# Kernel tuning notes

Hardware: AMD Instinct MI355X
Metric: run time of the kernel (lower is better)

Reference implementation:

```python
import jax, jax.numpy as jnp
import numpy as np

B, KPLUS1, D = 64, 513, 1024

def setup_inputs() -> dict:
    key = jax.random.key(0)
    k1, k2, k3 = jax.random.split(key, 3)
    x = jax.random.normal(k1, (B, KPLUS1, D), dtype=jnp.float32)
    # glorot-style scaled init for faithfulness in magnitude
    dense_weights = jax.random.normal(k2, (2 * D, D), dtype=jnp.float32) * (1.0 / np.sqrt(2 * D))
    dot_bias = jax.random.normal(k3, (D, 1), dtype=jnp.float32) * (1.0 / np.sqrt(D))
    return {"x": x, "dense_weights": dense_weights, "dot_bias": dot_bias}

def reference(x, dense_weights, dot_bias):
    # x: [B, K+1, D]; x[:,0] = sentence encoding u, x[:,1:] = knowledge z_t
    u = x[:, 0, :]            # [B, D]
    z = x[:, 1:, :]           # [B, K, D]
    d = z.shape[-1]
    # concat(z_t, u) @ W1 == z @ W1[:D] + u @ W1[D:], broadcast over K
    # (mathematically identical to the tile+concat+matmul in the original)
    w_z = dense_weights[:d, :]   # [D, D]
    w_u = dense_weights[d:, :]   # [D, D]
    m = jnp.tanh(jnp.einsum('bkd,de->bke', z, w_z)
                 + jnp.einsum('bd,de->be', u, w_u)[:, None, :])  # [B, K, D]
    q = jnp.einsum('bke,e->bk', m, dot_bias[:, 0])               # [B, K]
    return jax.nn.softmax(q, axis=-1)                            # [B, K]
```

## Files before the change

### kernel.cpp

```cpp
#include <hip/hip_runtime.h>
#include <hip/hip_bf16.h>


typedef __attribute__((ext_vector_type(8))) short short8;
typedef __attribute__((ext_vector_type(8))) _Float16 half8;
typedef __attribute__((ext_vector_type(4))) float f32x4;
typedef unsigned short ushort_t;

typedef const __attribute__((address_space(1))) void gvoid_t;
typedef __attribute__((address_space(3))) void lvoid_t;

__device__ __forceinline__ ushort_t f2bf(float f) {
    unsigned u = __float_as_uint(f);
    unsigned r = u + 0x7FFFu + ((u >> 16) & 1u);
    return (ushort_t)(r >> 16);
}
__device__ __forceinline__ float bf2f(ushort_t h) {
    return __uint_as_float(((unsigned)h) << 16);
}
__device__ __forceinline__ float tanh_fast(float x) {
    float e = __expf(2.f * x);
    return 1.f - 2.f / (e + 1.f);
}

__global__ __launch_bounds__(256) void k_prep_z16(const float* __restrict__ x,
                                                  _Float16* __restrict__ z_h) {
    const int idx8 = blockIdx.x * 256 + threadIdx.x;
    const int m = idx8 >> 7;
    const int c = (idx8 & 127) * 8;
    const int b = m >> 9, k = m & 511;
    const float* src = x + ((size_t)(b * 513 + 1 + k) << 10) + c;
    const float4 v0 = *(const float4*)src;
    const float4 v1 = *(const float4*)(src + 4);
    float vv[8] = {v0.x, v0.y, v0.z, v0.w, v1.x, v1.y, v1.z, v1.w};
    half8 hv;
#pragma unroll
    for (int i = 0; i < 8; ++i) hv[i] = (_Float16)vv[i];
    *(half8*)(z_h + (size_t)m * 1024 + c) = hv;
}

__global__ void k_prep_w16(const float* __restrict__ w,
                           _Float16* __restrict__ wzt) {
    __shared__ _Float16 th[64][66];
    const int k0 = blockIdx.x * 64;
    const int n0 = blockIdx.y * 64;
    const int t = threadIdx.x;
    const int lr = t >> 6;
    const int lc = t & 63;
#pragma unroll
    for (int r = 0; r < 16; ++r) {
        int kk = r * 4 + lr;
        th[kk][lc] = (_Float16)w[(size_t)(k0 + kk) * 1024 + n0 + lc];
    }
    __syncthreads();
#pragma unroll
    for (int r = 0; r < 16; ++r) {
        int nn = r * 4 + lr;
        wzt[(size_t)(n0 + nn) * 1024 + k0 + lc] = th[lc][nn];
    }
}

__global__ void k_hu(const float* __restrict__ x,
                     const float* __restrict__ w,
                     float* __restrict__ hu) {
    __shared__ float us[1024];
    const int b = blockIdx.y;
    const int e = blockIdx.x * 256 + threadIdx.x;
    for (int i = threadIdx.x; i < 1024; i += 256)
        us[i] = x[(size_t)b * 513 * 1024 + i];
    __syncthreads();
    const float* wu = w + (size_t)1024 * 1024;
    float acc = 0.f;
#pragma unroll 8
    for (int d = 0; d < 1024; ++d)
        acc = fmaf(us[d], wu[(size_t)d * 1024 + e], acc);
    hu[b * 1024 + e] = acc;
}

__global__ __launch_bounds__(512, 2) void k_gemm9(
        const _Float16* __restrict__ z_h,
        const _Float16* __restrict__ wzt,
        const float* __restrict__ hu,
        const float* __restrict__ bias,
        float* __restrict__ qp) {
    __shared__ __align__(16) _Float16 As[256 * 64];
    __shared__ __align__(16) _Float16 Bs[256 * 64];
    __shared__ float qred[2][4][128];

    const int t = threadIdx.x;
    const int mtile = blockIdx.x;
    const int ntile = blockIdx.y;
    const int wid = t >> 6;
    const int l = t & 63;
    const int wm = wid >> 2;
    const int wn = wid & 3;
    const int lr = l & 15;
    const int g = l >> 4;

    const int rl = l >> 3;
    const int chunk = (l & 7) ^ rl;
    const int w4 = wid & 3;
    const _Float16* gsrc;
    _Float16* ldsT;
    if (wid < 4) {
        gsrc = z_h + (size_t)(mtile * 256 + w4 * 64 + rl) * 1024 + chunk * 8;
        ldsT = As + w4 * 4096;
    } else {
        gsrc = wzt + (size_t)(ntile * 256 + w4 * 64 + rl) * 1024 + chunk * 8;
        ldsT = Bs + w4 * 4096;
    }

    f32x4 acc[8][4] = {};

    for (int k0 = 0; k0 < 1024; k0 += 64) {
#pragma unroll
        for (int j = 0; j < 8; ++j) {
            __builtin_amdgcn_global_load_lds(
                (gvoid_t*)(gsrc + k0 + j * 8192),
                (lvoid_t*)((char*)ldsT + j * 1024 + l * 16),
                16, 0, 0);
        }
        __syncthreads();

#pragma unroll
        for (int ks = 0; ks < 2; ++ks) {
            half8 afr[8], bfr[4];
            const int so = ((ks * 4 + g) ^ (lr & 7)) * 16;
#pragma unroll
            for (int ni = 0; ni < 4; ++ni)
                bfr[ni] = *(const half8*)((const char*)Bs + (wn * 64 + ni * 16 + lr) * 128 + so);
#pragma unroll
            for (int mi = 0; mi < 8; ++mi)
                afr[mi] = *(const half8*)((const char*)As + (wm * 128 + mi * 16 + lr) * 128 + so);
#pragma unroll
            for (int mi = 0; mi < 8; ++mi)
#pragma unroll
                for (int ni = 0; ni < 4; ++ni)
                    acc[mi][ni] = __builtin_amdgcn_mfma_f32_16x16x32_f16(
                        afr[mi], bfr[ni], acc[mi][ni], 0, 0, 0);
        }
        __syncthreads();
    }

    const int bb = mtile >> 1;
    float hu4[4], bias4[4];
#pragma unroll
    for (int ni = 0; ni < 4; ++ni) {
        int e = ntile * 256 + wn * 64 + ni * 16 + lr;
        hu4[ni] = hu[bb * 1024 + e];
        bias4[ni] = bias[e];
    }
#pragma unroll
    for (int mi = 0; mi < 8; ++mi) {
#pragma unroll
        for (int j = 0; j < 4; ++j) {
            float v = 0.f;
#pragma unroll
            for (int ni = 0; ni < 4; ++ni)
                v += tanh_fast(acc[mi][ni][j] + hu4[ni]) * bias4[ni];
            v += __shfl_xor(v, 1);
            v += __shfl_xor(v, 2);
            v += __shfl_xor(v, 4);
            v += __shfl_xor(v, 8);
            if (lr == 0)
                qred[wm][wn][mi * 16 + g * 4 + j] = v;
        }
    }
    __syncthreads();
    if (t < 256) {
        const int wmr = t >> 7;
        const int rr = t & 127;
        float q = qred[wmr][0][rr] + qred[wmr][1][rr]
                + qred[wmr][2][rr] + qred[wmr][3][rr];
        qp[(size_t)ntile * 32768 + mtile * 256 + t] = q;
    }
}

__global__ void k_prep_w(const float* __restrict__ w,
                         ushort_t* __restrict__ wzt_hi,
                         ushort_t* __restrict__ wzt_lo) {
    __shared__ ushort_t th[64][66];
    __shared__ ushort_t tl[64][66];
    const int k0 = blockIdx.x * 64;
    const int n0 = blockIdx.y * 64;
    const int t = threadIdx.x;
    const int lr = t >> 6;
    const int lc = t & 63;
#pragma unroll
    for (int r = 0; r < 16; ++r) {
        int kk = r * 4 + lr;
        float f = w[(size_t)(k0 + kk) * 1024 + n0 + lc];
        ushort_t hi = f2bf(f);
        ushort_t lo = f2bf(f - bf2f(hi));
        th[kk][lc] = hi;
        tl[kk][lc] = lo;
    }
    __syncthreads();
#pragma unroll
    for (int r = 0; r < 16; ++r) {
        int nn = r * 4 + lr;
        wzt_hi[(size_t)(n0 + nn) * 1024 + k0 + lc] = th[lc][nn];
        wzt_lo[(size_t)(n0 + nn) * 1024 + k0 + lc] = tl[lc][nn];
    }
}

__global__ __launch_bounds__(256) void k_gemm(
        const float* __restrict__ x,
        const ushort_t* __restrict__ wzt_hi,
        const ushort_t* __restrict__ wzt_lo,
        const float* __restrict__ hu,
        const float* __restrict__ bias,
        float* __restrict__ qp) {
    __shared__ ushort_t As_hi[128][40];
    __shared__ ushort_t As_lo[128][40];
    __shared__ ushort_t Bs_hi[128][40];
    __shared__ ushort_t Bs_lo[128][40];
    __shared__ float qred[2][2][64];

    const int t = threadIdx.x;
    const int mtile = blockIdx.x;
    const int ntile = blockIdx.y;
    const int wid = t >> 6;
    const int l = t & 63;
    const int wm = wid >> 1;
    const int wn = wid & 1;

    f32x4 acc[4][4] = {};

    const int arow = t >> 3;
    const int acol = (t & 7) * 4;
    size_t abase[4];
#pragma unroll
    for (int it = 0; it < 4; ++it) {
        int m = mtile * 128 + arow + it * 32;
        int bb = m >> 9;
        int kk = m & 511;
        abase[it] = ((size_t)(bb * 513 + 1 + kk)) * 1024 + acol;
    }
    const int brow = t >> 2;
    const int bcol = (t & 3) * 8;
    const size_t bbase = (size_t)(ntile * 128 + brow) * 1024 + bcol;

    for (int k0 = 0; k0 < 1024; k0 += 32) {
#pragma unroll
        for (int it = 0; it < 4; ++it) {
            const float4 v = *(const float4*)(x + abase[it] + k0);
            ushort4 hv, lv;
            hv.x = f2bf(v.x); lv.x = f2bf(v.x - bf2f(hv.x));
            hv.y = f2bf(v.y); lv.y = f2bf(v.y - bf2f(hv.y));
            hv.z = f2bf(v.z); lv.z = f2bf(v.z - bf2f(hv.z));
            hv.w = f2bf(v.w); lv.w = f2bf(v.w - bf2f(hv.w));
            const int row = arow + it * 32;
            *(ushort4*)&As_hi[row][acol] = hv;
            *(ushort4*)&As_lo[row][acol] = lv;
        }
#pragma unroll
        for (int it = 0; it < 2; ++it) {
            const int row = brow + it * 64;
            const uint4 vh = *(const uint4*)(wzt_hi + bbase + (size_t)it * 64 * 1024 + k0);
            const uint4 vl = *(const uint4*)(wzt_lo + bbase + (size_t)it * 64 * 1024 + k0);
            *(uint4*)&Bs_hi[row][bcol] = vh;
            *(uint4*)&Bs_lo[row][bcol] = vl;
        }
        __syncthreads();

        const int lr = l & 15;
        const int lk = (l >> 4) * 8;
        short8 ah[4], al[4], bh[4], bl[4];
#pragma unroll
        for (int i = 0; i < 4; ++i) {
            ah[i] = *(const short8*)&As_hi[wm * 64 + i * 16 + lr][lk];
            al[i] = *(const short8*)&As_lo[wm * 64 + i * 16 + lr][lk];
            bh[i] = *(const short8*)&Bs_hi[wn * 64 + i * 16 + lr][lk];
            bl[i] = *(const short8*)&Bs_lo[wn * 64 + i * 16 + lr][lk];
        }
#pragma unroll
        for (int mi = 0; mi < 4; ++mi)
#pragma unroll
            for (int ni = 0; ni < 4; ++ni) {
                acc[mi][ni] = __builtin_amdgcn_mfma_f32_16x16x32_bf16(ah[mi], bh[ni], acc[mi][ni], 0, 0, 0);
                acc[mi][ni] = __builtin_amdgcn_mfma_f32_16x16x32_bf16(ah[mi], bl[ni], acc[mi][ni], 0, 0, 0);
                acc[mi][ni] = __builtin_amdgcn_mfma_f32_16x16x32_bf16(al[mi], bh[ni], acc[mi][ni], 0, 0, 0);
            }
        __syncthreads();
    }

    const int lr = l & 15;
    const int lg = l >> 4;
    const int bbatch = mtile >> 2;
    float hu4[4], bias4[4];
#pragma unroll
    for (int ni = 0; ni < 4; ++ni) {
        int e = ntile * 128 + wn * 64 + ni * 16 + lr;
        hu4[ni] = hu[bbatch * 1024 + e];
        bias4[ni] = bias[e];
    }
#pragma unroll
    for (int mi = 0; mi < 4; ++mi) {
#pragma unroll
        for (int j = 0; j < 4; ++j) {
            float v = 0.f;
#pragma unroll
            for (int ni = 0; ni < 4; ++ni)
                v += tanhf(acc[mi][ni][j] + hu4[ni]) * bias4[ni];
            v += __shfl_xor(v, 1);
            v += __shfl_xor(v, 2);
            v += __shfl_xor(v, 4);
            v += __shfl_xor(v, 8);
            if (lr == 0)
                qred[wm][wn][mi * 16 + lg * 4 + j] = v;
        }
    }
    __syncthreads();
    if (t < 128) {
        const int wmr = t >> 6;
        const int rr = t & 63;
        float qv = qred[wmr][0][rr] + qred[wmr][1][rr];
        qp[(size_t)ntile * 32768 + mtile * 128 + t] = qv;
    }
}

__global__ void k_softmax(const float* __restrict__ qp, float* __restrict__ out,
                          int nt) {
    const int b = blockIdx.x;
    const int k = threadIdx.x;
    float q = 0.f;
    for (int i = 0; i < nt; ++i)
        q += qp[(size_t)i * 32768 + b * 512 + k];

    __shared__ float redm[8];
    __shared__ float reds[8];
    const int wid = k >> 6;

    float m = q;
#pragma unroll
    for (int off = 32; off >= 1; off >>= 1)
        m = fmaxf(m, __shfl_xor(m, off));
    if ((k & 63) == 0) redm[wid] = m;
    __syncthreads();
    m = redm[0];
#pragma unroll
    for (int i = 1; i < 8; ++i) m = fmaxf(m, redm[i]);

    float p = expf(q - m);
    float s = p;
#pragma unroll
    for (int off = 32; off >= 1; off >>= 1)
        s += __shfl_xor(s, off);
    if ((k & 63) == 0) reds[wid] = s;
    __syncthreads();
    s = 0.f;
#pragma unroll
    for (int i = 0; i < 8; ++i) s += reds[i];

    out[b * 512 + k] = p / s;
}

extern "C" void kernel_launch(void* const* d_in, const int* in_sizes, int n_in,
                              void* d_out, int out_size, void* d_ws, size_t ws_size,
                              hipStream_t stream) {
    const float* x    = (const float*)d_in[0];
    const float* w    = (const float*)d_in[1];
    const float* bias = (const float*)d_in[2];
    float* out = (float*)d_out;

    char* ws = (char*)d_ws;
    const size_t ZN = (size_t)32768 * 1024;

    const size_t need = ZN * sizeof(_Float16)
                      + (size_t)1024 * 1024 * sizeof(_Float16)
                      + (size_t)64 * 1024 * sizeof(float)
                      + (size_t)4 * 32768 * sizeof(float);

    if (ws_size >= need) {
        _Float16* z_h = (_Float16*)ws;
        _Float16* wzt = z_h + ZN;
        float*    hu  = (float*)(wzt + (size_t)1024 * 1024);
        float*    qp  = hu + (size_t)64 * 1024;

        k_prep_z16<<<16384, 256, 0, stream>>>(x, z_h);
        k_prep_w16<<<dim3(16, 16), 256, 0, stream>>>(w, wzt);
        k_hu<<<dim3(4, 64), 256, 0, stream>>>(x, w, hu);
        k_gemm9<<<dim3(128, 4), 512, 0, stream>>>(z_h, wzt, hu, bias, qp);
        k_softmax<<<64, 512, 0, stream>>>(qp, out, 4);
    } else {
        ushort_t* wzt_hi = (ushort_t*)ws;
        ushort_t* wzt_lo = wzt_hi + (size_t)1024 * 1024;
        float* hu = (float*)(ws + (size_t)4 * 1024 * 1024);
        float* qp = hu + (size_t)64 * 1024;

        k_prep_w<<<dim3(16, 16), 256, 0, stream>>>(w, wzt_hi, wzt_lo);
        k_hu<<<dim3(4, 64), 256, 0, stream>>>(x, w, hu);
        k_gemm<<<dim3(256, 8), 256, 0, stream>>>(x, wzt_hi, wzt_lo, hu, bias, qp);
        k_softmax<<<64, 512, 0, stream>>>(qp, out, 8);
    }
}
```

Before: 180.6 us.

## Fuse fp32-to-fp16 conversion of z into GEMM A-tile loading

```diff
diff --git a/kernel.cpp b/kernel.cpp
--- a/kernel.cpp
+++ b/kernel.cpp
@@ -21,22 +21,6 @@
 __device__ __forceinline__ float tanh_fast(float x) {
     float e = __expf(2.f * x);
     return 1.f - 2.f / (e + 1.f);
-}
-
-__global__ __launch_bounds__(256) void k_prep_z16(const float* __restrict__ x,
-                                                  _Float16* __restrict__ z_h) {
-    const int idx8 = blockIdx.x * 256 + threadIdx.x;
-    const int m = idx8 >> 7;
-    const int c = (idx8 & 127) * 8;
-    const int b = m >> 9, k = m & 511;
-    const float* src = x + ((size_t)(b * 513 + 1 + k) << 10) + c;
-    const float4 v0 = *(const float4*)src;
-    const float4 v1 = *(const float4*)(src + 4);
-    float vv[8] = {v0.x, v0.y, v0.z, v0.w, v1.x, v1.y, v1.z, v1.w};
-    half8 hv;
-#pragma unroll
-    for (int i = 0; i < 8; ++i) hv[i] = (_Float16)vv[i];
-    *(half8*)(z_h + (size_t)m * 1024 + c) = hv;
 }
 
 __global__ void k_prep_w16(const float* __restrict__ w,
@@ -77,8 +61,8 @@
     hu[b * 1024 + e] = acc;
 }
 
-__global__ __launch_bounds__(512, 2) void k_gemm9(
-        const _Float16* __restrict__ z_h,
+__global__ __launch_bounds__(512, 2) void k_gemm10(
+        const float* __restrict__ x,
         const _Float16* __restrict__ wzt,
         const float* __restrict__ hu,
         const float* __restrict__ bias,
@@ -97,28 +81,46 @@
     const int lr = l & 15;
     const int g = l >> 4;
 
-    const int rl = l >> 3;
-    const int chunk = (l & 7) ^ rl;
-    const int w4 = wid & 3;
-    const _Float16* gsrc;
-    _Float16* ldsT;
-    if (wid < 4) {
-        gsrc = z_h + (size_t)(mtile * 256 + w4 * 64 + rl) * 1024 + chunk * 8;
-        ldsT = As + w4 * 4096;
-    } else {
-        gsrc = wzt + (size_t)(ntile * 256 + w4 * 64 + rl) * 1024 + chunk * 8;
-        ldsT = Bs + w4 * 4096;
-    }
+    const int srow = t >> 3;
+    const int sphys = (t & 7) ^ (srow & 7);
+    const int schunk = sphys;
+    const int bb = mtile >> 1;
+    size_t aSrc[4];
+#pragma unroll
+    for (int j = 0; j < 4; ++j) {
+        int m = mtile * 256 + srow + j * 64;
+        int kk = m & 511;
+        aSrc[j] = ((size_t)(bb * 513 + 1 + kk) << 10) + (t & 7) * 8;
+    }
+    int aDst[4];
+#pragma unroll
+    for (int j = 0; j < 4; ++j)
+        aDst[j] = (srow + j * 64) * 128 + sphys * 16;
+    size_t bSrc[4];
+#pragma unroll
+    for (int j = 0; j < 4; ++j)
+        bSrc[j] = (size_t)(ntile * 256 + srow + j * 64) * 1024 + schunk * 8;
+    const int bDst0 = t * 16;
 
     f32x4 acc[8][4] = {};
 
     for (int k0 = 0; k0 < 1024; k0 += 64) {
 #pragma unroll
-        for (int j = 0; j < 8; ++j) {
+        for (int j = 0; j < 4; ++j) {
             __builtin_amdgcn_global_load_lds(
-                (gvoid_t*)(gsrc + k0 + j * 8192),
-                (lvoid_t*)((char*)ldsT + j * 1024 + l * 16),
-                16, 0, 0);
+                (gvoid_t*)(wzt + bSrc[j] + k0),
+                (lvoid_t*)((char*)Bs + j * 8192 + bDst0), 16, 0, 0);
+        }
+#pragma unroll
+        for (int j = 0; j < 4; ++j) {
+            const float4 v0 = *(const float4*)(x + aSrc[j] + k0);
+            const float4 v1 = *(const float4*)(x + aSrc[j] + k0 + 4);
+            half8 hv;
+            hv[0] = (_Float16)v0.x; hv[1] = (_Float16)v0.y;
+            hv[2] = (_Float16)v0.z; hv[3] = (_Float16)v0.w;
+            hv[4] = (_Float16)v1.x; hv[5] = (_Float16)v1.y;
+            hv[6] = (_Float16)v1.z; hv[7] = (_Float16)v1.w;
+            *(half8*)((char*)As + aDst[j]) = hv;
         }
         __syncthreads();
 
@@ -142,7 +144,6 @@
         __syncthreads();
     }
 
-    const int bb = mtile >> 1;
     float hu4[4], bias4[4];
 #pragma unroll
     for (int ni = 0; ni < 4; ++ni) {
@@ -365,23 +366,19 @@
     float* out = (float*)d_out;
 
     char* ws = (char*)d_ws;
-    const size_t ZN = (size_t)32768 * 1024;
-
-    const size_t need = ZN * sizeof(_Float16)
-                      + (size_t)1024 * 1024 * sizeof(_Float16)
+
+    const size_t need = (size_t)1024 * 1024 * sizeof(_Float16)
                       + (size_t)64 * 1024 * sizeof(float)
                       + (size_t)4 * 32768 * sizeof(float);
 
     if (ws_size >= need) {
-        _Float16* z_h = (_Float16*)ws;
-        _Float16* wzt = z_h + ZN;
+        _Float16* wzt = (_Float16*)ws;
         float*    hu  = (float*)(wzt + (size_t)1024 * 1024);
         float*    qp  = hu + (size_t)64 * 1024;
 
-        k_prep_z16<<<16384, 256, 0, stream>>>(x, z_h);
         k_prep_w16<<<dim3(16, 16), 256, 0, stream>>>(w, wzt);
         k_hu<<<dim3(4, 64), 256, 0, stream>>>(x, w, hu);
-        k_gemm9<<<dim3(128, 4), 512, 0, stream>>>(z_h, wzt, hu, bias, qp);
+        k_gemm10<<<dim3(128, 4), 512, 0, stream>>>(x, wzt, hu, bias, qp);
         k_softmax<<<64, 512, 0, stream>>>(qp, out, 4);
     } else {
         ushort_t* wzt_hi = (ushort_t*)ws;
```

After: 174.2 us. 1.04x faster.

## Drop LDS staging in fp16 GEMM and load MFMA fragments directly from global

Applied to the files above, without the earlier changes.

```diff
diff --git a/kernel.cpp b/kernel.cpp
--- a/kernel.cpp
+++ b/kernel.cpp
@@ -6,9 +6,6 @@
 typedef __attribute__((ext_vector_type(8))) _Float16 half8;
 typedef __attribute__((ext_vector_type(4))) float f32x4;
 typedef unsigned short ushort_t;
-
-typedef const __attribute__((address_space(1))) void gvoid_t;
-typedef __attribute__((address_space(3))) void lvoid_t;
 
 __device__ __forceinline__ ushort_t f2bf(float f) {
     unsigned u = __float_as_uint(f);
@@ -32,10 +29,11 @@
     const float* src = x + ((size_t)(b * 513 + 1 + k) << 10) + c;
     const float4 v0 = *(const float4*)src;
     const float4 v1 = *(const float4*)(src + 4);
-    float vv[8] = {v0.x, v0.y, v0.z, v0.w, v1.x, v1.y, v1.z, v1.w};
     half8 hv;
-#pragma unroll
-    for (int i = 0; i < 8; ++i) hv[i] = (_Float16)vv[i];
+    hv[0] = (_Float16)v0.x; hv[1] = (_Float16)v0.y;
+    hv[2] = (_Float16)v0.z; hv[3] = (_Float16)v0.w;
+    hv[4] = (_Float16)v1.x; hv[5] = (_Float16)v1.y;
+    hv[6] = (_Float16)v1.z; hv[7] = (_Float16)v1.w;
     *(half8*)(z_h + (size_t)m * 1024 + c) = hv;
 }
 
@@ -77,14 +75,12 @@
     hu[b * 1024 + e] = acc;
 }
 
-__global__ __launch_bounds__(512, 2) void k_gemm9(
+__global__ __launch_bounds__(512) void k_gemm14(
         const _Float16* __restrict__ z_h,
         const _Float16* __restrict__ wzt,
         const float* __restrict__ hu,
         const float* __restrict__ bias,
         float* __restrict__ qp) {
-    __shared__ __align__(16) _Float16 As[256 * 64];
-    __shared__ __align__(16) _Float16 Bs[256 * 64];
     __shared__ float qred[2][4][128];
 
     const int t = threadIdx.x;
@@ -97,49 +93,26 @@
     const int lr = l & 15;
     const int g = l >> 4;
 
-    const int rl = l >> 3;
-    const int chunk = (l & 7) ^ rl;
-    const int w4 = wid & 3;
-    const _Float16* gsrc;
-    _Float16* ldsT;
-    if (wid < 4) {
-        gsrc = z_h + (size_t)(mtile * 256 + w4 * 64 + rl) * 1024 + chunk * 8;
-        ldsT = As + w4 * 4096;
-    } else {
-        gsrc = wzt + (size_t)(ntile * 256 + w4 * 64 + rl) * 1024 + chunk * 8;
-        ldsT = Bs + w4 * 4096;
-    }
+    const _Float16* aBase = z_h + (size_t)(mtile * 256 + wm * 128 + lr) * 1024 + g * 8;
+    const _Float16* bBase = wzt + (size_t)(ntile * 256 + wn * 64 + lr) * 1024 + g * 8;
 
     f32x4 acc[8][4] = {};
 
-    for (int k0 = 0; k0 < 1024; k0 += 64) {
-#pragma unroll
-        for (int j = 0; j < 8; ++j) {
-            __builtin_amdgcn_global_load_lds(
-                (gvoid_t*)(gsrc + k0 + j * 8192),
-                (lvoid_t*)((char*)ldsT + j * 1024 + l * 16),
-                16, 0, 0);
-        }
-        __syncthreads();
-
-#pragma unroll
-        for (int ks = 0; ks < 2; ++ks) {
-            half8 afr[8], bfr[4];
-            const int so = ((ks * 4 + g) ^ (lr & 7)) * 16;
+#pragma unroll 4
+    for (int k0 = 0; k0 < 1024; k0 += 32) {
+        half8 afr[8], bfr[4];
+#pragma unroll
+        for (int ni = 0; ni < 4; ++ni)
+            bfr[ni] = *(const half8*)(bBase + ni * 16384 + k0);
+#pragma unroll
+        for (int mi = 0; mi < 8; ++mi)
+            afr[mi] = *(const half8*)(aBase + mi * 16384 + k0);
+#pragma unroll
+        for (int mi = 0; mi < 8; ++mi)
 #pragma unroll
             for (int ni = 0; ni < 4; ++ni)
-                bfr[ni] = *(const half8*)((const char*)Bs + (wn * 64 + ni * 16 + lr) * 128 + so);
-#pragma unroll
-            for (int mi = 0; mi < 8; ++mi)
-                afr[mi] = *(const half8*)((const char*)As + (wm * 128 + mi * 16 + lr) * 128 + so);
-#pragma unroll
-            for (int mi = 0; mi < 8; ++mi)
-#pragma unroll
-                for (int ni = 0; ni < 4; ++ni)
-                    acc[mi][ni] = __builtin_amdgcn_mfma_f32_16x16x32_f16(
-                        afr[mi], bfr[ni], acc[mi][ni], 0, 0, 0);
-        }
-        __syncthreads();
+                acc[mi][ni] = __builtin_amdgcn_mfma_f32_16x16x32_f16(
+                    afr[mi], bfr[ni], acc[mi][ni], 0, 0, 0);
     }
 
     const int bb = mtile >> 1;
@@ -381,7 +354,7 @@
         k_prep_z16<<<16384, 256, 0, stream>>>(x, z_h);
         k_prep_w16<<<dim3(16, 16), 256, 0, stream>>>(w, wzt);
         k_hu<<<dim3(4, 64), 256, 0, stream>>>(x, w, hu);
-        k_gemm9<<<dim3(128, 4), 512, 0, stream>>>(z_h, wzt, hu, bias, qp);
+        k_gemm14<<<dim3(128, 4), 512, 0, stream>>>(z_h, wzt, hu, bias, qp);
         k_softmax<<<64, 512, 0, stream>>>(qp, out, 4);
     } else {
         ushort_t* wzt_hi = (ushort_t*)ws;
```

After: 283.6 us. +57.0%, slower.
